# Performance work log

Hardware: AMD Instinct MI355X
Metric: run time of the kernel (lower is better)

## Reference

```python
import jax, jax.numpy as jnp
import numpy as np

N_NODES = 100000
D_FEAT = 256
HIDDEN1 = 128
HIDDEN2 = 64
N_EDGES = 1600000


def spmm(edge_src, edge_dst, edge_weight, h, n_nodes):
    # sparse adj @ h via gather + weighted segment-sum
    msgs = edge_weight[:, None] * h[edge_src]            # [E, F]
    return jax.ops.segment_sum(msgs, edge_dst, num_segments=n_nodes)


def setup_inputs() -> dict:
    key = jax.random.key(0)
    k1, k2, k3, k4, k5, k6 = jax.random.split(key, 6)
    x = jax.random.normal(k1, (N_NODES, D_FEAT), dtype=jnp.float32)
    edge_src = jax.random.randint(k2, (N_EDGES,), 0, N_NODES, dtype=jnp.int64)
    edge_dst = jax.random.randint(k3, (N_EDGES,), 0, N_NODES, dtype=jnp.int64)
    edge_weight = jax.random.uniform(k4, (N_EDGES,), dtype=jnp.float32)
    # Glorot-style init for layer weights
    W0 = jax.random.normal(k5, (D_FEAT, HIDDEN1), dtype=jnp.float32) * (1.0 / np.sqrt(D_FEAT))
    W1 = jax.random.normal(k6, (HIDDEN1, HIDDEN2), dtype=jnp.float32) * (1.0 / np.sqrt(HIDDEN1))
    return {"x": x, "edge_src": edge_src, "edge_dst": edge_dst,
            "edge_weight": edge_weight, "W0": W0, "W1": W1}


def reference(x, edge_src, edge_dst, edge_weight, W0, W1):
    n = x.shape[0]
    # layer 1: relu(adj @ (X @ W0))
    h1 = jax.nn.relu(spmm(edge_src, edge_dst, edge_weight, x @ W0, n))   # [N, H1]
    # layer 2: relu(adj @ (h1 @ W1))
    h2 = jax.nn.relu(spmm(edge_src, edge_dst, edge_weight, h1 @ W1, n))  # [N, H2]
    # final softmax over class/hidden2 dim (intended semantics of nn.Softmax)
    return jax.nn.softmax(h2, axis=-1)
```

## Files before the change

### kernel.cpp

```cpp
#include <hip/hip_runtime.h>
#include <hip/hip_bf16.h>

#define D_FEAT 256
#define H1 128
#define H2 64

typedef __attribute__((ext_vector_type(8))) short short8;
typedef __attribute__((ext_vector_type(4))) float f32x4;

__device__ __forceinline__ unsigned short f2b(float f) {
    __hip_bfloat16 b = __float2bfloat16(f);
    return *reinterpret_cast<unsigned short*>(&b);
}
__device__ __forceinline__ float b2f(unsigned short u) {
    return __uint_as_float((unsigned)u << 16);
}
__device__ __forceinline__ float blo(unsigned u) { return __uint_as_float(u << 16); }
__device__ __forceinline__ float bhi(unsigned u) { return __uint_as_float(u & 0xffff0000u); }

__global__ __launch_bounds__(256)
void conv_weights_split(const float* __restrict__ W0, const float* __restrict__ W1,
                        unsigned short* __restrict__ w0h, unsigned short* __restrict__ w0l,
                        unsigned short* __restrict__ w1h, unsigned short* __restrict__ w1l)
{
    const int t = blockIdx.x*256 + threadIdx.x;
    if (t < D_FEAT*H1) {
        const int col = t >> 8, k = t & 255;
        const float v = W0[(size_t)k*H1 + col];
        const unsigned short h = f2b(v);
        w0h[t] = h; w0l[t] = f2b(v - b2f(h));
    } else if (t < D_FEAT*H1 + H1*H2) {
        const int u = t - D_FEAT*H1;
        const int col = u >> 7, k = u & 127;
        const float v = W1[(size_t)k*H2 + col];
        const unsigned short h = f2b(v);
        w1h[u] = h; w1l[u] = f2b(v - b2f(h));
    }
}

__global__ __launch_bounds__(256)
void gemm1_mfma(const float* __restrict__ X,
                const unsigned short* __restrict__ W0H, const unsigned short* __restrict__ W0L,
                unsigned short* __restrict__ H0, int M)
{
    __shared__ unsigned short Ah[64*64], Al[64*64];
    __shared__ unsigned short Bh[128*64], Bl[128*64];
    const int tid = threadIdx.x;
    const int w = tid >> 6, l = tid & 63;
    const int lr = l & 15, lk = l >> 4;
    const int row0 = blockIdx.x * 64;

    f32x4 acc[8];
#pragma unroll
    for (int i = 0; i < 8; ++i) acc[i] = (f32x4){0.f, 0.f, 0.f, 0.f};

    for (int k0 = 0; k0 < D_FEAT; k0 += 64) {
#pragma unroll
        for (int c = tid; c < 512; c += 256) {
            const int r = c >> 3, kb = c & 7;
            int gr = row0 + r; gr = gr < M ? gr : M - 1;
            const float4 f0 = *(const float4*)&X[(size_t)gr*D_FEAT + k0 + kb*8];
            const float4 f1 = *(const float4*)&X[(size_t)gr*D_FEAT + k0 + kb*8 + 4];
            const float v[8] = {f0.x,f0.y,f0.z,f0.w,f1.x,f1.y,f1.z,f1.w};
            unsigned short hh[8], ll[8];
#pragma unroll
            for (int j = 0; j < 8; ++j) {
                hh[j] = f2b(v[j]);
                ll[j] = f2b(v[j] - b2f(hh[j]));
            }
            uint4 ph, pl;
            ph.x = hh[0] | ((unsigned)hh[1] << 16); ph.y = hh[2] | ((unsigned)hh[3] << 16);
            ph.z = hh[4] | ((unsigned)hh[5] << 16); ph.w = hh[6] | ((unsigned)hh[7] << 16);
            pl.x = ll[0] | ((unsigned)ll[1] << 16); pl.y = ll[2] | ((unsigned)ll[3] << 16);
            pl.z = ll[4] | ((unsigned)ll[5] << 16); pl.w = ll[6] | ((unsigned)ll[7] << 16);
            const int o = r*64 + ((kb ^ (r & 7)) << 3);
            *(uint4*)&Ah[o] = ph;
            *(uint4*)&Al[o] = pl;
        }
#pragma unroll
        for (int c = tid; c < 1024; c += 256) {
            const int col = c >> 3, kb = c & 7;
            const size_t gsrc = (size_t)col*D_FEAT + k0 + kb*8;
            const int o = col*64 + ((kb ^ (col & 7)) << 3);
            *(uint4*)&Bh[o] = *(const uint4*)&W0H[gsrc];
            *(uint4*)&Bl[o] = *(const uint4*)&W0L[gsrc];
        }
        __syncthreads();
#pragma unroll
        for (int sub = 0; sub < 2; ++sub) {
            const int ar = 16*w + lr;
            const int ao = ar*64 + (((sub*4 + lk) ^ (ar & 7)) << 3);
            const short8 ah = *(const short8*)&Ah[ao];
            const short8 al = *(const short8*)&Al[ao];
#pragma unroll
            for (int ct = 0; ct < 8; ++ct) {
                const int col = ct*16 + lr;
                const int bo = col*64 + (((sub*4 + lk) ^ (col & 7)) << 3);
                const short8 bh = *(const short8*)&Bh[bo];
                const short8 bl = *(const short8*)&Bl[bo];
                acc[ct] = __builtin_amdgcn_mfma_f32_16x16x32_bf16(ah, bh, acc[ct], 0, 0, 0);
                acc[ct] = __builtin_amdgcn_mfma_f32_16x16x32_bf16(al, bh, acc[ct], 0, 0, 0);
                acc[ct] = __builtin_amdgcn_mfma_f32_16x16x32_bf16(ah, bl, acc[ct], 0, 0, 0);
            }
        }
        __syncthreads();
    }
#pragma unroll
    for (int ct = 0; ct < 8; ++ct) {
#pragma unroll
        for (int r = 0; r < 4; ++r) {
            const int row = row0 + 16*w + 4*lk + r;
            if (row < M) H0[(size_t)row*H1 + ct*16 + lr] = f2b(acc[ct][r]);
        }
    }
}

__global__ __launch_bounds__(256)
void gemm2_mfma(const float* __restrict__ S1,
                const unsigned short* __restrict__ W1H, const unsigned short* __restrict__ W1L,
                float* __restrict__ H1W, int M)
{
    __shared__ unsigned short Ah[64*64], Al[64*64];
    __shared__ unsigned short Bh[64*64], Bl[64*64];
    const int tid = threadIdx.x;
    const int w = tid >> 6, l = tid & 63;
    const int lr = l & 15, lk = l >> 4;
    const int row0 = blockIdx.x * 64;

    f32x4 acc[4];
#pragma unroll
    for (int i = 0; i < 4; ++i) acc[i] = (f32x4){0.f, 0.f, 0.f, 0.f};

    for (int k0 = 0; k0 < H1; k0 += 64) {
#pragma unroll
        for (int c = tid; c < 512; c += 256) {
            const int r = c >> 3, kb = c & 7;
            int gr = row0 + r; gr = gr < M ? gr : M - 1;
            const float4 f0 = *(const float4*)&S1[(size_t)gr*H1 + k0 + kb*8];
            const float4 f1 = *(const float4*)&S1[(size_t)gr*H1 + k0 + kb*8 + 4];
            const float v[8] = {f0.x,f0.y,f0.z,f0.w,f1.x,f1.y,f1.z,f1.w};
            unsigned short hh[8], ll[8];
#pragma unroll
            for (int j = 0; j < 8; ++j) {
                hh[j] = f2b(v[j]);
                ll[j] = f2b(v[j] - b2f(hh[j]));
            }
            uint4 ph, pl;
            ph.x = hh[0] | ((unsigned)hh[1] << 16); ph.y = hh[2] | ((unsigned)hh[3] << 16);
            ph.z = hh[4] | ((unsigned)hh[5] << 16); ph.w = hh[6] | ((unsigned)hh[7] << 16);
            pl.x = ll[0] | ((unsigned)ll[1] << 16); pl.y = ll[2] | ((unsigned)ll[3] << 16);
            pl.z = ll[4] | ((unsigned)ll[5] << 16); pl.w = ll[6] | ((unsigned)ll[7] << 16);
            const int o = r*64 + ((kb ^ (r & 7)) << 3);
            *(uint4*)&Ah[o] = ph;
            *(uint4*)&Al[o] = pl;
        }
#pragma unroll
        for (int c = tid; c < 512; c += 256) {
            const int col = c >> 3, kb = c & 7;
            const size_t gsrc = (size_t)col*H1 + k0 + kb*8;
            const int o = col*64 + ((kb ^ (col & 7)) << 3);
            *(uint4*)&Bh[o] = *(const uint4*)&W1H[gsrc];
            *(uint4*)&Bl[o] = *(const uint4*)&W1L[gsrc];
        }
        __syncthreads();
#pragma unroll
        for (int sub = 0; sub < 2; ++sub) {
            const int ar = 16*w + lr;
            const int ao = ar*64 + (((sub*4 + lk) ^ (ar & 7)) << 3);
            const short8 ah = *(const short8*)&Ah[ao];
            const short8 al = *(const short8*)&Al[ao];
#pragma unroll
            for (int ct = 0; ct < 4; ++ct) {
                const int col = ct*16 + lr;
                const int bo = col*64 + (((sub*4 + lk) ^ (col & 7)) << 3);
                const short8 bh = *(const short8*)&Bh[bo];
                const short8 bl = *(const short8*)&Bl[bo];
                acc[ct] = __builtin_amdgcn_mfma_f32_16x16x32_bf16(ah, bh, acc[ct], 0, 0, 0);
                acc[ct] = __builtin_amdgcn_mfma_f32_16x16x32_bf16(al, bh, acc[ct], 0, 0, 0);
                acc[ct] = __builtin_amdgcn_mfma_f32_16x16x32_bf16(ah, bl, acc[ct], 0, 0, 0);
            }
        }
        __syncthreads();
    }
#pragma unroll
    for (int ct = 0; ct < 4; ++ct) {
#pragma unroll
        for (int r = 0; r < 4; ++r) {
            const int row = row0 + 16*w + 4*lk + r;
            if (row < M) H1W[(size_t)row*H2 + ct*16 + lr] = acc[ct][r];
        }
    }
}

__global__ __launch_bounds__(256)
void hist_dst(const int* __restrict__ dst, int* __restrict__ cnt, int E)
{
    const int e = blockIdx.x*256 + threadIdx.x;
    if (e < E) atomicAdd(&cnt[dst[e]], 1);
}

__global__ __launch_bounds__(256)
void scan_partial(const int* __restrict__ in, int* __restrict__ out,
                  int* __restrict__ bsums, int n)
{
    const int gid  = blockIdx.x*256 + threadIdx.x;
    const int lane = threadIdx.x & 63;
    const int wv   = threadIdx.x >> 6;
    const int v = (gid < n) ? in[gid] : 0;
    int s = v;
#pragma unroll
    for (int off = 1; off < 64; off <<= 1) {
        const int u = __shfl_up(s, off);
        if (lane >= off) s += u;
    }
    __shared__ int ws[4];
    if (lane == 63) ws[wv] = s;
    __syncthreads();
    int add = 0;
#pragma unroll
    for (int i = 0; i < 4; ++i) if (i < wv) add += ws[i];
    s += add;
    if (gid < n) out[gid] = s - v;
    if (threadIdx.x == 255) bsums[blockIdx.x] = s;
}

__global__ __launch_bounds__(1024)
void scan_bsums(int* __restrict__ bs, int nb)
{
    __shared__ int buf[1024];
    const int t = threadIdx.x;
    const int v = (t < nb) ? bs[t] : 0;
    buf[t] = v;
    __syncthreads();
    for (int off = 1; off < 1024; off <<= 1) {
        const int u = (t >= off) ? buf[t-off] : 0;
        __syncthreads();
        buf[t] += u;
        __syncthreads();
    }
    if (t < nb) bs[t] = buf[t] - v;
}

__global__ __launch_bounds__(256)
void scan_add(int* __restrict__ out, const int* __restrict__ bs, int n, int total)
{
    const int gid = blockIdx.x*256 + threadIdx.x;
    if (gid < n) out[gid] += bs[blockIdx.x];
    if (gid == 0) out[n] = total;
}

__global__ __launch_bounds__(256)
void scatter_edges(const int* __restrict__ src, const int* __restrict__ dst,
                   const float* __restrict__ w, int* __restrict__ cur,
                   int2* __restrict__ recs, int E)
{
    const int e = blockIdx.x*256 + threadIdx.x;
    if (e < E) {
        const int p = atomicAdd(&cur[dst[e]], 1);
        recs[p] = make_int2(src[e], __float_as_int(w[e]));
    }
}

__global__ __launch_bounds__(256)
void spmm1_b16(const int2* __restrict__ recs, const int* __restrict__ rp,
               const unsigned short* __restrict__ h, float* __restrict__ out, int N)
{
    const int gtid = blockIdx.x*256 + threadIdx.x;
    const int node = gtid >> 4;
    if (node >= N) return;
    const int lane = threadIdx.x & 15;
    const int off  = lane * 8;
    const int s = rp[node], e = rp[node+1];

    float acc[8] = {0.f,0.f,0.f,0.f,0.f,0.f,0.f,0.f};
    int i = s;
    for (; i + 1 < e; i += 2) {
        const int2 r0 = recs[i], r1 = recs[i+1];
        const uint4 v0 = *(const uint4*)&h[(size_t)r0.x*H1 + off];
        const uint4 v1 = *(const uint4*)&h[(size_t)r1.x*H1 + off];
        const float w0 = __int_as_float(r0.y), w1 = __int_as_float(r1.y);
        acc[0] = fmaf(w0, blo(v0.x), acc[0]); acc[1] = fmaf(w0, bhi(v0.x), acc[1]);
        acc[2] = fmaf(w0, blo(v0.y), acc[2]); acc[3] = fmaf(w0, bhi(v0.y), acc[3]);
        acc[4] = fmaf(w0, blo(v0.z), acc[4]); acc[5] = fmaf(w0, bhi(v0.z), acc[5]);
        acc[6] = fmaf(w0, blo(v0.w), acc[6]); acc[7] = fmaf(w0, bhi(v0.w), acc[7]);
        acc[0] = fmaf(w1, blo(v1.x), acc[0]); acc[1] = fmaf(w1, bhi(v1.x), acc[1]);
        acc[2] = fmaf(w1, blo(v1.y), acc[2]); acc[3] = fmaf(w1, bhi(v1.y), acc[3]);
        acc[4] = fmaf(w1, blo(v1.z), acc[4]); acc[5] = fmaf(w1, bhi(v1.z), acc[5]);
        acc[6] = fmaf(w1, blo(v1.w), acc[6]); acc[7] = fmaf(w1, bhi(v1.w), acc[7]);
    }
    if (i < e) {
        const int2 r = recs[i];
        const uint4 v = *(const uint4*)&h[(size_t)r.x*H1 + off];
        const float w0 = __int_as_float(r.y);
        acc[0] = fmaf(w0, blo(v.x), acc[0]); acc[1] = fmaf(w0, bhi(v.x), acc[1]);
        acc[2] = fmaf(w0, blo(v.y), acc[2]); acc[3] = fmaf(w0, bhi(v.y), acc[3]);
        acc[4] = fmaf(w0, blo(v.z), acc[4]); acc[5] = fmaf(w0, bhi(v.z), acc[5]);
        acc[6] = fmaf(w0, blo(v.w), acc[6]); acc[7] = fmaf(w0, bhi(v.w), acc[7]);
    }
    float4 o0, o1;
    o0.x = fmaxf(acc[0],0.f); o0.y = fmaxf(acc[1],0.f);
    o0.z = fmaxf(acc[2],0.f); o0.w = fmaxf(acc[3],0.f);
    o1.x = fmaxf(acc[4],0.f); o1.y = fmaxf(acc[5],0.f);
    o1.z = fmaxf(acc[6],0.f); o1.w = fmaxf(acc[7],0.f);
    *(float4*)&out[(size_t)node*H1 + off]     = o0;
    *(float4*)&out[(size_t)node*H1 + off + 4] = o1;
}

__global__ __launch_bounds__(256)
void spmm2_f32(const int2* __restrict__ recs, const int* __restrict__ rp,
               const float* __restrict__ h, float* __restrict__ out, int N)
{
    const int gtid = blockIdx.x*256 + threadIdx.x;
    const int node = gtid >> 4;
    if (node >= N) return;
    const int lane = threadIdx.x & 15;
    const int off  = lane * 4;
    const int s = rp[node], e = rp[node+1];

    float ax = 0.f, ay = 0.f, az = 0.f, aw = 0.f;
    int i = s;
    for (; i + 1 < e; i += 2) {
        const int2 r0 = recs[i], r1 = recs[i+1];
        const float4 v0 = *(const float4*)(h + (size_t)r0.x*H2 + off);
        const float4 v1 = *(const float4*)(h + (size_t)r1.x*H2 + off);
        const float w0 = __int_as_float(r0.y), w1 = __int_as_float(r1.y);
        ax = fmaf(w0, v0.x, ax); ay = fmaf(w0, v0.y, ay);
        az = fmaf(w0, v0.z, az); aw = fmaf(w0, v0.w, aw);
        ax = fmaf(w1, v1.x, ax); ay = fmaf(w1, v1.y, ay);
        az = fmaf(w1, v1.z, az); aw = fmaf(w1, v1.w, aw);
    }
    if (i < e) {
        const int2 r = recs[i];
        const float4 v = *(const float4*)(h + (size_t)r.x*H2 + off);
        const float w0 = __int_as_float(r.y);
        ax = fmaf(w0, v.x, ax); ay = fmaf(w0, v.y, ay);
        az = fmaf(w0, v.z, az); aw = fmaf(w0, v.w, aw);
    }
    float4 o; o.x = ax; o.y = ay; o.z = az; o.w = aw;
    *(float4*)(out + (size_t)node*H2 + off) = o;
}

__global__ __launch_bounds__(256)
void relu_softmax64(float* __restrict__ io, int M)
{
    const int row  = blockIdx.x*4 + (threadIdx.x >> 6);
    const int lane = threadIdx.x & 63;
    if (row >= M) return;
    float v = io[(size_t)row*64 + lane];
    v = fmaxf(v, 0.f);
    float m = v;
#pragma unroll
    for (int off = 32; off >= 1; off >>= 1) m = fmaxf(m, __shfl_xor(m, off));
    const float e = __expf(v - m);
    float s = e;
#pragma unroll
    for (int off = 32; off >= 1; off >>= 1) s += __shfl_xor(s, off);
    io[(size_t)row*64 + lane] = e / s;
}

extern "C" void kernel_launch(void* const* d_in, const int* in_sizes, int n_in,
                              void* d_out, int out_size, void* d_ws, size_t ws_size,
                              hipStream_t stream)
{
    const float* x    = (const float*)d_in[0];
    const int*   esrc = (const int*)  d_in[1];
    const int*   edst = (const int*)  d_in[2];
    const float* ew   = (const float*)d_in[3];
    const float* W0   = (const float*)d_in[4];
    const float* W1   = (const float*)d_in[5];

    const int N = in_sizes[0] / D_FEAT;
    const int E = in_sizes[1];

    unsigned short* h0   = (unsigned short*)d_ws;
    float*          s1   = (float*)(h0 + (size_t)N*H1);
    int2*           recs = (int2*)(s1 + (size_t)N*H1);
    int*            rp   = (int*)(recs + E);
    unsigned short* w0h  = (unsigned short*)(((uintptr_t)(rp + N + 1) + 63) & ~(uintptr_t)63);
    unsigned short* w0l  = w0h + D_FEAT*H1;
    unsigned short* w1h  = w0l + D_FEAT*H1;
    unsigned short* w1l  = w1h + H1*H2;
    int* cnt = (int*)d_ws;
    int* cur = cnt + N;
    int* bs  = cur + N;
    float* h1w = (float*)d_ws;
    float* out = (float*)d_out;

    conv_weights_split<<<(D_FEAT*H1 + H1*H2 + 255)/256, 256, 0, stream>>>(
        W0, W1, w0h, w0l, w1h, w1l);

    hipMemsetAsync(cnt, 0, (size_t)N*sizeof(int), stream);
    hist_dst<<<(E+255)/256, 256, 0, stream>>>(edst, cnt, E);
    const int nb = (N+255)/256;
    scan_partial<<<nb, 256, 0, stream>>>(cnt, rp, bs, N);
    scan_bsums<<<1, 1024, 0, stream>>>(bs, nb);
    scan_add<<<nb, 256, 0, stream>>>(rp, bs, N, E);
    hipMemcpyAsync(cur, rp, (size_t)N*sizeof(int), hipMemcpyDeviceToDevice, stream);
    scatter_edges<<<(E+255)/256, 256, 0, stream>>>(esrc, edst, ew, cur, recs, E);

    gemm1_mfma<<<(N+63)/64, 256, 0, stream>>>(x, w0h, w0l, h0, N);
    spmm1_b16<<<(N*16+255)/256, 256, 0, stream>>>(recs, rp, h0, s1, N);

    gemm2_mfma<<<(N+63)/64, 256, 0, stream>>>(s1, w1h, w1l, h1w, N);
    spmm2_f32<<<(N*16+255)/256, 256, 0, stream>>>(recs, rp, h1w, out, N);

    relu_softmax64<<<(N+3)/4, 256, 0, stream>>>(out, N);
}
```

Measured before the change: 538.9 us.

## Pack edge records into 32 bits, unroll SpMM by four, fuse relu-softmax

Each edge record shrinks from an int2 (source index plus fp32 weight) to one 32-bit word: the source index in the upper 17 bits and the weight as a truncated 15-bit bf16 with no sign bit, which only works because weights are non-negative and below 2^17 nodes. The layer-2 SpMM now applies ReLU and the row softmax in registers with 16-lane shuffles, so the separate softmax kernel and its extra read and write of the output are gone. Both SpMM gather loops are unrolled to four edges to keep more loads in flight. Storing weights in bf16 lowers precision, and the packing depends on the input ranges.

New measurement: 496.6 us. 7.9% less time.

```diff
diff --git a/kernel.cpp b/kernel.cpp
--- a/kernel.cpp
+++ b/kernel.cpp
@@ -252,17 +252,21 @@
 __global__ __launch_bounds__(256)
 void scatter_edges(const int* __restrict__ src, const int* __restrict__ dst,
                    const float* __restrict__ w, int* __restrict__ cur,
-                   int2* __restrict__ recs, int E)
+                   unsigned* __restrict__ recs, int E)
 {
     const int e = blockIdx.x*256 + threadIdx.x;
     if (e < E) {
         const int p = atomicAdd(&cur[dst[e]], 1);
-        recs[p] = make_int2(src[e], __float_as_int(w[e]));
-    }
-}
-
-__global__ __launch_bounds__(256)
-void spmm1_b16(const int2* __restrict__ recs, const int* __restrict__ rp,
+        recs[p] = ((unsigned)src[e] << 15) | (unsigned)f2b(w[e]);
+    }
+}
+
+#define UNPACK(rec, sidx, wt) \
+    const unsigned sidx = (rec) >> 15; \
+    const float wt = __uint_as_float(((rec) & 0x7fffu) << 16);
+
+__global__ __launch_bounds__(256)
+void spmm1_b16(const unsigned* __restrict__ recs, const int* __restrict__ rp,
                const unsigned short* __restrict__ h, float* __restrict__ out, int N)
 {
     const int gtid = blockIdx.x*256 + threadIdx.x;
@@ -273,30 +277,31 @@
     const int s = rp[node], e = rp[node+1];
 
     float acc[8] = {0.f,0.f,0.f,0.f,0.f,0.f,0.f,0.f};
+
+#define ACC1(v, wt) \
+    acc[0] = fmaf(wt, blo(v.x), acc[0]); acc[1] = fmaf(wt, bhi(v.x), acc[1]); \
+    acc[2] = fmaf(wt, blo(v.y), acc[2]); acc[3] = fmaf(wt, bhi(v.y), acc[3]); \
+    acc[4] = fmaf(wt, blo(v.z), acc[4]); acc[5] = fmaf(wt, bhi(v.z), acc[5]); \
+    acc[6] = fmaf(wt, blo(v.w), acc[6]); acc[7] = fmaf(wt, bhi(v.w), acc[7]);
+
     int i = s;
-    for (; i + 1 < e; i += 2) {
-        const int2 r0 = recs[i], r1 = recs[i+1];
-        const uint4 v0 = *(const uint4*)&h[(size_t)r0.x*H1 + off];
-        const uint4 v1 = *(const uint4*)&h[(size_t)r1.x*H1 + off];
-        const float w0 = __int_as_float(r0.y), w1 = __int_as_float(r1.y);
-        acc[0] = fmaf(w0, blo(v0.x), acc[0]); acc[1] = fmaf(w0, bhi(v0.x), acc[1]);
-        acc[2] = fmaf(w0, blo(v0.y), acc[2]); acc[3] = fmaf(w0, bhi(v0.y), acc[3]);
-        acc[4] = fmaf(w0, blo(v0.z), acc[4]); acc[5] = fmaf(w0, bhi(v0.z), acc[5]);
-        acc[6] = fmaf(w0, blo(v0.w), acc[6]); acc[7] = fmaf(w0, bhi(v0.w), acc[7]);
-        acc[0] = fmaf(w1, blo(v1.x), acc[0]); acc[1] = fmaf(w1, bhi(v1.x), acc[1]);
-        acc[2] = fmaf(w1, blo(v1.y), acc[2]); acc[3] = fmaf(w1, bhi(v1.y), acc[3]);
-        acc[4] = fmaf(w1, blo(v1.z), acc[4]); acc[5] = fmaf(w1, bhi(v1.z), acc[5]);
-        acc[6] = fmaf(w1, blo(v1.w), acc[6]); acc[7] = fmaf(w1, bhi(v1.w), acc[7]);
-    }
-    if (i < e) {
-        const int2 r = recs[i];
-        const uint4 v = *(const uint4*)&h[(size_t)r.x*H1 + off];
-        const float w0 = __int_as_float(r.y);
-        acc[0] = fmaf(w0, blo(v.x), acc[0]); acc[1] = fmaf(w0, bhi(v.x), acc[1]);
-        acc[2] = fmaf(w0, blo(v.y), acc[2]); acc[3] = fmaf(w0, bhi(v.y), acc[3]);
-        acc[4] = fmaf(w0, blo(v.z), acc[4]); acc[5] = fmaf(w0, bhi(v.z), acc[5]);
-        acc[6] = fmaf(w0, blo(v.w), acc[6]); acc[7] = fmaf(w0, bhi(v.w), acc[7]);
-    }
+    for (; i + 3 < e; i += 4) {
+        const unsigned r0 = recs[i], r1 = recs[i+1], r2 = recs[i+2], r3 = recs[i+3];
+        UNPACK(r0, s0, w0) UNPACK(r1, s1, w1) UNPACK(r2, s2, w2) UNPACK(r3, s3, w3)
+        const uint4 v0 = *(const uint4*)&h[(size_t)s0*H1 + off];
+        const uint4 v1 = *(const uint4*)&h[(size_t)s1*H1 + off];
+        const uint4 v2 = *(const uint4*)&h[(size_t)s2*H1 + off];
+        const uint4 v3 = *(const uint4*)&h[(size_t)s3*H1 + off];
+        ACC1(v0, w0) ACC1(v1, w1) ACC1(v2, w2) ACC1(v3, w3)
+    }
+    for (; i < e; ++i) {
+        const unsigned r = recs[i];
+        UNPACK(r, s0, w0)
+        const uint4 v = *(const uint4*)&h[(size_t)s0*H1 + off];
+        ACC1(v, w0)
+    }
+#undef ACC1
+
     float4 o0, o1;
     o0.x = fmaxf(acc[0],0.f); o0.y = fmaxf(acc[1],0.f);
     o0.z = fmaxf(acc[2],0.f); o0.w = fmaxf(acc[3],0.f);
@@ -307,8 +312,8 @@
 }
 
 __global__ __launch_bounds__(256)
-void spmm2_f32(const int2* __restrict__ recs, const int* __restrict__ rp,
-               const float* __restrict__ h, float* __restrict__ out, int N)
+void spmm2_sm(const unsigned* __restrict__ recs, const int* __restrict__ rp,
+              const float* __restrict__ h, float* __restrict__ out, int N)
 {
     const int gtid = blockIdx.x*256 + threadIdx.x;
     const int node = gtid >> 4;
@@ -318,44 +323,42 @@
     const int s = rp[node], e = rp[node+1];
 
     float ax = 0.f, ay = 0.f, az = 0.f, aw = 0.f;
+
+#define ACC2(v, wt) \
+    ax = fmaf(wt, v.x, ax); ay = fmaf(wt, v.y, ay); \
+    az = fmaf(wt, v.z, az); aw = fmaf(wt, v.w, aw);
+
     int i = s;
-    for (; i + 1 < e; i += 2) {
-        const int2 r0 = recs[i], r1 = recs[i+1];
-        const float4 v0 = *(const float4*)(h + (size_t)r0.x*H2 + off);
-        const float4 v1 = *(const float4*)(h + (size_t)r1.x*H2 + off);
-        const float w0 = __int_as_float(r0.y), w1 = __int_as_float(r1.y);
-        ax = fmaf(w0, v0.x, ax); ay = fmaf(w0, v0.y, ay);
-        az = fmaf(w0, v0.z, az); aw = fmaf(w0, v0.w, aw);
-        ax = fmaf(w1, v1.x, ax); ay = fmaf(w1, v1.y, ay);
-        az = fmaf(w1, v1.z, az); aw = fmaf(w1, v1.w, aw);
-    }
-    if (i < e) {
-        const int2 r = recs[i];
-        const float4 v = *(const float4*)(h + (size_t)r.x*H2 + off);
-        const float w0 = __int_as_float(r.y);
-        ax = fmaf(w0, v.x, ax); ay = fmaf(w0, v.y, ay);
-        az = fmaf(w0, v.z, az); aw = fmaf(w0, v.w, aw);
-    }
-    float4 o; o.x = ax; o.y = ay; o.z = az; o.w = aw;
-    *(float4*)(out + (size_t)node*H2 + off) = o;
-}
-
-__global__ __launch_bounds__(256)
-void relu_softmax64(float* __restrict__ io, int M)
-{
-    const int row  = blockIdx.x*4 + (threadIdx.x >> 6);
-    const int lane = threadIdx.x & 63;
-    if (row >= M) return;
-    float v = io[(size_t)row*64 + lane];
-    v = fmaxf(v, 0.f);
-    float m = v;
-#pragma unroll
-    for (int off = 32; off >= 1; off >>= 1) m = fmaxf(m, __shfl_xor(m, off));
-    const float e = __expf(v - m);
-    float s = e;
-#pragma unroll
-    for (int off = 32; off >= 1; off >>= 1) s += __shfl_xor(s, off);
-    io[(size_t)row*64 + lane] = e / s;
+    for (; i + 3 < e; i += 4) {
+        const unsigned r0 = recs[i], r1 = recs[i+1], r2 = recs[i+2], r3 = recs[i+3];
+        UNPACK(r0, s0, w0) UNPACK(r1, s1, w1) UNPACK(r2, s2, w2) UNPACK(r3, s3, w3)
+        const float4 v0 = *(const float4*)(h + (size_t)s0*H2 + off);
+        const float4 v1 = *(const float4*)(h + (size_t)s1*H2 + off);
+        const float4 v2 = *(const float4*)(h + (size_t)s2*H2 + off);
+        const float4 v3 = *(const float4*)(h + (size_t)s3*H2 + off);
+        ACC2(v0, w0) ACC2(v1, w1) ACC2(v2, w2) ACC2(v3, w3)
+    }
+    for (; i < e; ++i) {
+        const unsigned r = recs[i];
+        UNPACK(r, s0, w0)
+        const float4 v = *(const float4*)(h + (size_t)s0*H2 + off);
+        ACC2(v, w0)
+    }
+#undef ACC2
+
+    ax = fmaxf(ax, 0.f); ay = fmaxf(ay, 0.f);
+    az = fmaxf(az, 0.f); aw = fmaxf(aw, 0.f);
+    float m = fmaxf(fmaxf(ax, ay), fmaxf(az, aw));
+#pragma unroll
+    for (int o = 8; o >= 1; o >>= 1) m = fmaxf(m, __shfl_xor(m, o));
+    const float ex = __expf(ax - m), ey = __expf(ay - m);
+    const float ez = __expf(az - m), ew2 = __expf(aw - m);
+    float sm = ex + ey + ez + ew2;
+#pragma unroll
+    for (int o = 8; o >= 1; o >>= 1) sm += __shfl_xor(sm, o);
+    const float inv = 1.f / sm;
+    float4 o4; o4.x = ex*inv; o4.y = ey*inv; o4.z = ez*inv; o4.w = ew2*inv;
+    *(float4*)(out + (size_t)node*H2 + off) = o4;
 }
 
 extern "C" void kernel_launch(void* const* d_in, const int* in_sizes, int n_in,
@@ -374,7 +377,7 @@
 
     unsigned short* h0   = (unsigned short*)d_ws;
     float*          s1   = (float*)(h0 + (size_t)N*H1);
-    int2*           recs = (int2*)(s1 + (size_t)N*H1);
+    unsigned*       recs = (unsigned*)(s1 + (size_t)N*H1);
     int*            rp   = (int*)(recs + E);
     unsigned short* w0h  = (unsigned short*)(((uintptr_t)(rp + N + 1) + 63) & ~(uintptr_t)63);
     unsigned short* w0l  = w0h + D_FEAT*H1;
@@ -402,7 +405,5 @@
     spmm1_b16<<<(N*16+255)/256, 256, 0, stream>>>(recs, rp, h0, s1, N);
 
     gemm2_mfma<<<(N+63)/64, 256, 0, stream>>>(s1, w1h, w1l, h1w, N);
-    spmm2_f32<<<(N*16+255)/256, 256, 0, stream>>>(recs, rp, h1w, out, N);
-
-    relu_softmax64<<<(N+3)/4, 256, 0, stream>>>(out, N);
-}
+    spmm2_sm<<<(N*16+255)/256, 256, 0, stream>>>(recs, rp, h1w, out, N);
+}
```
